# Optimization experiments

Hardware: AMD Instinct MI355X
Metric: run time of the kernel (lower is better)

## Reference

```python
import jax, jax.numpy as jnp
import numpy as np

DIM = 256
B = 8
H = 56
W = 56
K = 2
EPS = 1e-5  # torch BatchNorm2d default eps


def _conv1x1(x, w, b):
    # x: [B,C,H,W], w: [O,C], b: [O]
    return jnp.einsum('oc,bchw->bohw', w, x) + b[None, :, None, None]


def _bn(x, g, be, m, v):
    # inference-mode BatchNorm2d with running stats
    s = g / jnp.sqrt(v + EPS)
    return x * s[None, :, None, None] + (be - m * s)[None, :, None, None]


def _grapher(x, w1, b1, g1, be1, m1, v1, wg, bg, gg, beg, mg, vg, w2, b2, g2, be2, m2, v2):
    # fc1: 1x1 conv + BN
    h = _bn(_conv1x1(x, w1, b1), g1, be1, m1, v1)
    Hh, Ww = h.shape[2], h.shape[3]
    # MRConv4d: running max over circular-shift differences
    # torch.cat([x[:,:,-i:,:], x[:,:,:-i,:]], dim=2) == jnp.roll(x, i, axis=2)
    xj = jnp.zeros_like(h)

    def body_h(c, i):
        return jnp.maximum(c, h - jnp.roll(h, i, axis=2)), None

    xj, _ = jax.lax.scan(body_h, xj, jnp.arange(K, Hh, K))

    def body_w(c, i):
        return jnp.maximum(c, h - jnp.roll(h, i, axis=3)), None

    xj, _ = jax.lax.scan(body_w, xj, jnp.arange(K, Ww, K))

    cat = jnp.concatenate([h, xj], axis=1)  # [B, 2*dim, H, W]
    # MRConv4d.nn: Conv2d(2*dim, 2*dim, 1) -> BN(2*dim) -> GELU (exact erf)
    g = jax.nn.gelu(_bn(_conv1x1(cat, wg, bg), gg, beg, mg, vg), approximate=False)
    # fc2: Conv2d(2*dim, dim, 1) + BN(dim), then residual
    return _bn(_conv1x1(g, w2, b2), g2, be2, m2, v2) + x


def setup_inputs() -> dict:
    key = jax.random.key(0)
    ks = jax.random.split(key, 12)
    d, d2 = DIM, 2 * DIM

    def w(k, o, c):
        return jax.random.normal(k, (o, c), jnp.float32) * np.float32(1.0 / np.sqrt(c))

    return {
        'x': jax.random.normal(ks[0], (B, d, H, W), jnp.float32),
        'w1': w(ks[1], d, d), 'b1': jnp.zeros((d,), jnp.float32),
        'g1': jnp.ones((d,), jnp.float32), 'be1': jnp.zeros((d,), jnp.float32),
        'm1': jax.random.normal(ks[2], (d,), jnp.float32) * 0.1,
        'v1': jax.random.uniform(ks[3], (d,), jnp.float32, 0.5, 1.5),
        'wg': w(ks[4], d2, d2), 'bg': jnp.zeros((d2,), jnp.float32),
        'gg': jnp.ones((d2,), jnp.float32), 'beg': jnp.zeros((d2,), jnp.float32),
        'mg': jax.random.normal(ks[5], (d2,), jnp.float32) * 0.1,
        'vg': jax.random.uniform(ks[6], (d2,), jnp.float32, 0.5, 1.5),
        'w2': w(ks[7], d, d2), 'b2': jnp.zeros((d,), jnp.float32),
        'g2': jnp.ones((d,), jnp.float32), 'be2': jnp.zeros((d,), jnp.float32),
        'm2': jax.random.normal(ks[8], (d,), jnp.float32) * 0.1,
        'v2': jax.random.uniform(ks[9], (d,), jnp.float32, 0.5, 1.5),
    }


def reference(x, w1, b1, g1, be1, m1, v1, wg, bg, gg, beg, mg, vg, w2, b2, g2, be2, m2, v2):
    return _grapher(x, w1, b1, g1, be1, m1, v1, wg, bg, gg, beg, mg, vg, w2, b2, g2, be2, m2, v2)
```

## Files before the change

### kernel.cpp

```cpp
#include <hip/hip_runtime.h>
#include <math.h>

#define SPB 3136
#define NB 8
#define MTOT (NB*SPB)
#define EPS 1e-5f
#define XT_LD  288
#define CAT_LD 544

typedef unsigned short u16;
typedef __attribute__((ext_vector_type(8))) short short8;
typedef __attribute__((ext_vector_type(4))) float float4v;

__device__ __forceinline__ float b2f(u16 v){ unsigned u=((unsigned)v)<<16; float f; __builtin_memcpy(&f,&u,4); return f; }
__device__ __forceinline__ u16 f2b(float f){ unsigned u; __builtin_memcpy(&u,&f,4); u += 0x7fffu + ((u>>16)&1u); return (u16)(u>>16); }
__device__ __forceinline__ float gelu_f(float z){
  float t = 1.5957691216f * z * (1.0f + 0.044715f*z*z);
  return __fdividef(z, 1.0f + __expf(-t));
}

__device__ __forceinline__ void gll16(const u16* g, u16* l){
  __builtin_amdgcn_global_load_lds((const __attribute__((address_space(1))) void*)g,
                                   (__attribute__((address_space(3))) void*)l, 16, 0, 0);
}

__global__ void prep_k(const float* __restrict__ x, u16* __restrict__ xt,
                       const float* __restrict__ w1,const float* __restrict__ wg,const float* __restrict__ w2,
                       const float* b1,const float* g1,const float* be1,const float* m1,const float* v1,
                       const float* bg,const float* gg,const float* beg,const float* mg,const float* vg,
                       const float* b2,const float* g2,const float* be2,const float* m2,const float* v2,
                       u16* __restrict__ w1b,u16* __restrict__ wgb,u16* __restrict__ w2b,float* cst){
  __shared__ float t[32][33];
  if (blockIdx.z < 8) {
    int b = blockIdx.z, ct = blockIdx.y, st = blockIdx.x;
    int ts = threadIdx.x, tc = threadIdx.y;
    #pragma unroll
    for (int i=0;i<4;i++){
      int c = tc + i*8;
      t[c][ts] = x[((size_t)(b*256 + ct*32 + c))*SPB + st*32 + ts];
    }
    __syncthreads();
    #pragma unroll
    for (int i=0;i<4;i++){
      int r = tc + i*8;
      xt[((size_t)(b*SPB + st*32 + r))*XT_LD + ct*32 + ts] = f2b(t[ts][r]);
    }
  } else {
    int tid = threadIdx.y*32 + threadIdx.x;
    int w = ((blockIdx.z-8)*8 + blockIdx.y)*98 + blockIdx.x;
    int i = w*256 + tid;
    if (i < 65536)  w1b[(i>>8)*XT_LD  + (i&255)] = f2b(w1[i]);
    if (i < 262144) wgb[(i>>9)*CAT_LD + (i&511)] = f2b(wg[i]);
    if (i < 131072) w2b[(i>>9)*CAT_LD + (i&511)] = f2b(w2[i]);
    if (i < 256) {
      float s = g1[i]*rsqrtf(v1[i]+EPS);
      cst[i] = s; cst[256+i] = b1[i]*s + be1[i] - m1[i]*s;
      float s2 = g2[i]*rsqrtf(v2[i]+EPS);
      cst[1536+i] = s2; cst[1792+i] = b2[i]*s2 + be2[i] - m2[i]*s2;
    }
    if (i < 512) {
      float s = gg[i]*rsqrtf(vg[i]+EPS);
      cst[512+i] = s; cst[1024+i] = bg[i]*s + beg[i] - mg[i]*s;
    }
  }
}

__global__ __launch_bounds__(256) void minmax_k(const u16* __restrict__ cat, float* __restrict__ rmin, float* __restrict__ cmin){
  __shared__ float red[8][256];
  int b = blockIdx.x/56, i = blockIdx.x%56;
  int col = blockIdx.y;
  int slice = threadIdx.x >> 5;
  int c0 = (threadIdx.x & 31) * 8;
  const u16* base; size_t stride;
  if (!col){ base = cat + ((size_t)(b*SPB + i*56))*CAT_LD + c0; stride = CAT_LD; }
  else     { base = cat + ((size_t)(b*SPB + i))*CAT_LD + c0;    stride = (size_t)56*CAT_LD; }
  float m[8];
  #pragma unroll
  for (int k=0;k<8;k++) m[k]=3.4e38f;
  #pragma unroll
  for (int jj=0;jj<7;jj++){
    short8 v = *(const short8*)(base + (size_t)(slice + jj*8)*stride);
    #pragma unroll
    for (int k=0;k<8;k++) m[k] = fminf(m[k], b2f((u16)v[k]));
  }
  #pragma unroll
  for (int k=0;k<8;k++) red[slice][c0+k] = m[k];
  __syncthreads();
  int t = threadIdx.x;
  if (t < 64){
    int par = t >> 5;
    int cc = (t & 31) * 8;
    float* out = col ? cmin : rmin;
    float* p = &out[((size_t)(b*2+par)*56 + i)*256 + cc];
    #pragma unroll
    for (int k=0;k<8;k++)
      p[k] = fminf(fminf(red[par][cc+k], red[par+2][cc+k]),
                   fminf(red[par+4][cc+k], red[par+6][cc+k]));
  }
}

__global__ __launch_bounds__(256) void xj_k(u16* __restrict__ cat, const float* __restrict__ rmin, const float* __restrict__ cmin){
  int b = blockIdx.y;
  int t = threadIdx.x;
  int s = blockIdx.x*8 + (t>>5);
  int c0 = (t&31)*8;
  int y = s/56, x = s%56;
  size_t idx = ((size_t)(b*SPB + s))*CAT_LD;
  short8 h8 = *(const short8*)&cat[idx + c0];
  const float* cp = &cmin[((size_t)(b*2+(y&1))*56 + x)*256 + c0];
  const float* rp = &rmin[((size_t)(b*2+(x&1))*56 + y)*256 + c0];
  float4v cv0 = *(const float4v*)cp, cv1 = *(const float4v*)(cp+4);
  float4v rv0 = *(const float4v*)rp, rv1 = *(const float4v*)(rp+4);
  short8 o;
  #pragma unroll
  for (int j=0;j<8;j++){
    float cm = (j<4) ? cv0[j] : cv1[j-4];
    float rm = (j<4) ? rv0[j] : rv1[j-4];
    o[j] = (short)f2b(fmaxf(0.0f, b2f((u16)h8[j]) - fminf(cm, rm)));
  }
  *(short8*)&cat[idx + 256 + c0] = o;
}

__device__ __forceinline__ int xcd_remap(int orig, int nwg){
  int q = nwg >> 3, r = nwg & 7, xc = orig & 7, rest = orig >> 3;
  int base = (xc < r) ? xc*(q+1) : r*(q+1) + (xc-r)*q;
  return base + rest;
}

template<int KTOT, int LDA, int LDB, int EPI>
__global__ __launch_bounds__(256,2) void gemm_k(
    const u16* __restrict__ Ain, const u16* __restrict__ Wt,
    const float* __restrict__ scale, const float* __restrict__ bias,
    void* __restrict__ outp, const float* __restrict__ resid)
{
  __shared__ __align__(16) u16 smem[36864];
  const int tid = threadIdx.x;
  const int nwg = gridDim.x * gridDim.y;
  const int flat = blockIdx.y * gridDim.x + blockIdx.x;
  const int s_ = xcd_remap(flat, nwg);
  const int m0 = (s_ / gridDim.y) * 256;
  const int o0 = (s_ % gridDim.y) * 128;
  const int lane = tid & 63, wid = tid >> 6;
  const int quad = lane >> 4, l16 = lane & 15;

  float4v acc[4][8];
  #pragma unroll
  for (int i=0;i<4;i++)
    #pragma unroll
    for (int j=0;j<8;j++) acc[i][j] = (float4v){0.f,0.f,0.f,0.f};

  const int row = tid >> 2;
  const int q8s = ((tid & 3) ^ ((tid >> 3) & 3)) * 8;
  const u16* ga0 = Ain + ((size_t)(m0 + row))*LDA + q8s;
  const u16* gb0 = Wt  + ((size_t)(o0 + row))*LDB + q8s;
  u16* l8 = smem + tid*8;

  auto STAGE = [&](int kt, int buf){
    u16* b_ = l8 + buf*12288;
    gll16(ga0 + kt,                     b_);
    gll16(ga0 + (size_t) 64*LDA + kt,   b_ + 2048);
    gll16(ga0 + (size_t)128*LDA + kt,   b_ + 4096);
    gll16(ga0 + (size_t)192*LDA + kt,   b_ + 6144);
    gll16(gb0 + kt,                     b_ + 8192);
    gll16(gb0 + (size_t) 64*LDB + kt,   b_ + 10240);
  };
  const int swz = (l16 >> 1) & 3;
  auto COMPUTE = [&](int buf){
    const u16* A_ = smem + buf*12288;
    const u16* B_ = A_ + 8192;
    const int kq = (quad ^ swz) * 8;
    short8 af[4], bfr[8];
    #pragma unroll
    for (int im=0;im<4;im++) af[im]  = *(const short8*)&A_[(wid*64+im*16+l16)*32 + kq];
    #pragma unroll
    for (int in=0;in<8;in++) bfr[in] = *(const short8*)&B_[(in*16+l16)*32 + kq];
    #pragma unroll
    for (int im=0;im<4;im++)
      #pragma unroll
      for (int in=0;in<8;in++)
        acc[im][in] = __builtin_amdgcn_mfma_f32_16x16x32_bf16(af[im], bfr[in], acc[im][in], 0, 0, 0);
  };

  constexpr int NIT = KTOT / 32;
  STAGE(0, 0);
  STAGE(32, 1);
  #pragma unroll
  for (int t = 0; t < NIT; ++t) {
    __builtin_amdgcn_sched_barrier(0);
    if (t + 1 < NIT) asm volatile("s_waitcnt vmcnt(6) lgkmcnt(0)" ::: "memory");
    else             asm volatile("s_waitcnt vmcnt(0) lgkmcnt(0)" ::: "memory");
    __builtin_amdgcn_s_barrier();
    __builtin_amdgcn_sched_barrier(0);
    if (t + 2 < NIT) STAGE((t+2)*32, (t+2)%3);
    COMPUTE(t%3);
  }
  __syncthreads();

  if (EPI == 1 || EPI == 2) {
    u16* tile = smem;
    #pragma unroll
    for (int im=0;im<4;im++)
      #pragma unroll
      for (int in=0;in<8;in++){
        int ol = in*16 + l16;
        float sc = scale[o0+ol], bi = bias[o0+ol];
        #pragma unroll
        for (int r=0;r<4;r++){
          float v = acc[im][in][r]*sc + bi;
          if (EPI==2) v = gelu_f(v);
          tile[(wid*64+im*16+quad*4+r)*128 + ol] = f2b(v);
        }
      }
    __syncthreads();
    u16* op = (u16*)outp;
    #pragma unroll
    for (int p=0;p<16;p++){
      int chunk = p*256 + tid;
      int rr = chunk >> 4, off = (chunk & 15)*8;
      *(uint4*)&op[((size_t)(m0 + rr))*CAT_LD + o0 + off] = *(const uint4*)&tile[rr*128 + off];
    }
  } else {
    float* ftile = (float*)smem;
    float* op = (float*)outp;
    #pragma unroll
    for (int h=0; h<2; h++){
      #pragma unroll
      for (int im=0;im<4;im++)
        #pragma unroll
        for (int in4=0;in4<4;in4++){
          int in = h*4 + in4;
          int c64 = in4*16 + l16;
          int og = o0 + h*64 + c64;
          float sc = scale[og], bi = bias[og];
          float4v v;
          #pragma unroll
          for (int r=0;r<4;r++) v[r] = acc[im][in][r]*sc + bi;
          *(float4v*)&ftile[c64*260 + wid*64 + im*16 + quad*4] = v;
        }
      __syncthreads();
      #pragma unroll
      for (int p=0;p<16;p++){
        int chunk = p*256 + tid;
        int rr = chunk >> 6, off = (chunk & 63)*4;
        int m = m0 + off;
        int b = m / SPB, s = m - b*SPB;
        size_t g = ((size_t)(b*256 + o0 + h*64 + rr))*SPB + s;
        float4v v = *(const float4v*)&ftile[rr*260 + off];
        v.x += resid[g]; v.y += resid[g+1]; v.z += resid[g+2]; v.w += resid[g+3];
        *(float4v*)&op[g] = v;
      }
      __syncthreads();
    }
  }
}

extern "C" void kernel_launch(void* const* d_in, const int* in_sizes, int n_in,
                              void* d_out, int out_size, void* d_ws, size_t ws_size,
                              hipStream_t stream)
{
  const float* x  = (const float*)d_in[0];
  const float* w1 = (const float*)d_in[1];
  const float* b1 = (const float*)d_in[2];
  const float* g1 = (const float*)d_in[3];
  const float* be1= (const float*)d_in[4];
  const float* m1 = (const float*)d_in[5];
  const float* v1 = (const float*)d_in[6];
  const float* wg = (const float*)d_in[7];
  const float* bg = (const float*)d_in[8];
  const float* gg = (const float*)d_in[9];
  const float* beg= (const float*)d_in[10];
  const float* mg = (const float*)d_in[11];
  const float* vg = (const float*)d_in[12];
  const float* w2 = (const float*)d_in[13];
  const float* b2 = (const float*)d_in[14];
  const float* g2 = (const float*)d_in[15];
  const float* be2= (const float*)d_in[16];
  const float* m2 = (const float*)d_in[17];
  const float* v2 = (const float*)d_in[18];

  char* ws = (char*)d_ws;
  size_t off = 0;
  auto alloc = [&](size_t bytes){ void* p = ws + off; off += (bytes + 255) & ~(size_t)255; return p; };
  u16* xt    = (u16*)alloc((size_t)MTOT*XT_LD*2);
  u16* catt  = (u16*)alloc((size_t)MTOT*CAT_LD*2);
  u16* gt    = (u16*)alloc((size_t)MTOT*CAT_LD*2);
  u16* w1b   = (u16*)alloc((size_t)256*XT_LD*2);
  u16* wgb   = (u16*)alloc((size_t)512*CAT_LD*2);
  u16* w2b   = (u16*)alloc((size_t)256*CAT_LD*2);
  float* cst = (float*)alloc((size_t)2048*4);
  float* rmin= (float*)alloc((size_t)NB*2*56*256*4);
  float* cmin= (float*)alloc((size_t)NB*2*56*256*4);

  hipLaunchKernelGGL(prep_k, dim3(98,8,10), dim3(32,8), 0, stream,
                     x, xt, w1,wg,w2, b1,g1,be1,m1,v1, bg,gg,beg,mg,vg, b2,g2,be2,m2,v2,
                     w1b,wgb,w2b, cst);
  hipLaunchKernelGGL((gemm_k<256,XT_LD,XT_LD,1>), dim3(98,2), dim3(256), 0, stream,
                     xt, w1b, cst+0, cst+256, (void*)catt, (const float*)nullptr);
  hipLaunchKernelGGL(minmax_k, dim3(NB*56,2), dim3(256), 0, stream, catt, rmin, cmin);
  hipLaunchKernelGGL(xj_k, dim3(392, NB), dim3(256), 0, stream, catt, rmin, cmin);
  hipLaunchKernelGGL((gemm_k<512,CAT_LD,CAT_LD,2>), dim3(98,4), dim3(256), 0, stream,
                     catt, wgb, cst+512, cst+1024, (void*)gt, (const float*)nullptr);
  hipLaunchKernelGGL((gemm_k<512,CAT_LD,CAT_LD,3>), dim3(98,2), dim3(256), 0, stream,
                     gt, w2b, cst+1536, cst+1792, d_out, x);
}
```

Measured before the change: 179.4 us.

## Shrink GEMM tile to 128x128 with 512-thread blocks and 16-row warp slices

```diff
diff --git a/kernel.cpp b/kernel.cpp
--- a/kernel.cpp
+++ b/kernel.cpp
@@ -128,26 +128,24 @@
 }
 
 template<int KTOT, int LDA, int LDB, int EPI>
-__global__ __launch_bounds__(256,2) void gemm_k(
+__global__ __launch_bounds__(512,4) void gemm_k(
     const u16* __restrict__ Ain, const u16* __restrict__ Wt,
     const float* __restrict__ scale, const float* __restrict__ bias,
     void* __restrict__ outp, const float* __restrict__ resid)
 {
-  __shared__ __align__(16) u16 smem[36864];
+  __shared__ __align__(16) u16 smem[24576];
   const int tid = threadIdx.x;
   const int nwg = gridDim.x * gridDim.y;
   const int flat = blockIdx.y * gridDim.x + blockIdx.x;
   const int s_ = xcd_remap(flat, nwg);
-  const int m0 = (s_ / gridDim.y) * 256;
+  const int m0 = (s_ / gridDim.y) * 128;
   const int o0 = (s_ % gridDim.y) * 128;
   const int lane = tid & 63, wid = tid >> 6;
   const int quad = lane >> 4, l16 = lane & 15;
 
-  float4v acc[4][8];
-  #pragma unroll
-  for (int i=0;i<4;i++)
-    #pragma unroll
-    for (int j=0;j<8;j++) acc[i][j] = (float4v){0.f,0.f,0.f,0.f};
+  float4v acc[8];
+  #pragma unroll
+  for (int j=0;j<8;j++) acc[j] = (float4v){0.f,0.f,0.f,0.f};
 
   const int row = tid >> 2;
   const int q8s = ((tid & 3) ^ ((tid >> 3) & 3)) * 8;
@@ -156,29 +154,22 @@
   u16* l8 = smem + tid*8;
 
   auto STAGE = [&](int kt, int buf){
-    u16* b_ = l8 + buf*12288;
-    gll16(ga0 + kt,                     b_);
-    gll16(ga0 + (size_t) 64*LDA + kt,   b_ + 2048);
-    gll16(ga0 + (size_t)128*LDA + kt,   b_ + 4096);
-    gll16(ga0 + (size_t)192*LDA + kt,   b_ + 6144);
-    gll16(gb0 + kt,                     b_ + 8192);
-    gll16(gb0 + (size_t) 64*LDB + kt,   b_ + 10240);
+    u16* b_ = l8 + buf*8192;
+    gll16(ga0 + kt, b_);
+    gll16(gb0 + kt, b_ + 4096);
   };
   const int swz = (l16 >> 1) & 3;
   auto COMPUTE = [&](int buf){
-    const u16* A_ = smem + buf*12288;
-    const u16* B_ = A_ + 8192;
+    const u16* A_ = smem + buf*8192;
+    const u16* B_ = A_ + 4096;
     const int kq = (quad ^ swz) * 8;
-    short8 af[4], bfr[8];
-    #pragma unroll
-    for (int im=0;im<4;im++) af[im]  = *(const short8*)&A_[(wid*64+im*16+l16)*32 + kq];
+    short8 af = *(const short8*)&A_[(wid*16 + l16)*32 + kq];
+    short8 bfr[8];
     #pragma unroll
     for (int in=0;in<8;in++) bfr[in] = *(const short8*)&B_[(in*16+l16)*32 + kq];
     #pragma unroll
-    for (int im=0;im<4;im++)
-      #pragma unroll
-      for (int in=0;in<8;in++)
-        acc[im][in] = __builtin_amdgcn_mfma_f32_16x16x32_bf16(af[im], bfr[in], acc[im][in], 0, 0, 0);
+    for (int in=0;in<8;in++)
+      acc[in] = __builtin_amdgcn_mfma_f32_16x16x32_bf16(af, bfr[in], acc[in], 0, 0, 0);
   };
 
   constexpr int NIT = KTOT / 32;
@@ -187,7 +178,7 @@
   #pragma unroll
   for (int t = 0; t < NIT; ++t) {
     __builtin_amdgcn_sched_barrier(0);
-    if (t + 1 < NIT) asm volatile("s_waitcnt vmcnt(6) lgkmcnt(0)" ::: "memory");
+    if (t + 1 < NIT) asm volatile("s_waitcnt vmcnt(2) lgkmcnt(0)" ::: "memory");
     else             asm volatile("s_waitcnt vmcnt(0) lgkmcnt(0)" ::: "memory");
     __builtin_amdgcn_s_barrier();
     __builtin_amdgcn_sched_barrier(0);
@@ -199,23 +190,21 @@
   if (EPI == 1 || EPI == 2) {
     u16* tile = smem;
     #pragma unroll
-    for (int im=0;im<4;im++)
+    for (int in=0;in<8;in++){
+      int ol = in*16 + l16;
+      float sc = scale[o0+ol], bi = bias[o0+ol];
       #pragma unroll
-      for (int in=0;in<8;in++){
-        int ol = in*16 + l16;
-        float sc = scale[o0+ol], bi = bias[o0+ol];
-        #pragma unroll
-        for (int r=0;r<4;r++){
-          float v = acc[im][in][r]*sc + bi;
-          if (EPI==2) v = gelu_f(v);
-          tile[(wid*64+im*16+quad*4+r)*128 + ol] = f2b(v);
-        }
+      for (int r=0;r<4;r++){
+        float v = acc[in][r]*sc + bi;
+        if (EPI==2) v = gelu_f(v);
+        tile[(wid*16+quad*4+r)*128 + ol] = f2b(v);
       }
+    }
     __syncthreads();
     u16* op = (u16*)outp;
     #pragma unroll
-    for (int p=0;p<16;p++){
-      int chunk = p*256 + tid;
+    for (int p=0;p<4;p++){
+      int chunk = p*512 + tid;
       int rr = chunk >> 4, off = (chunk & 15)*8;
       *(uint4*)&op[((size_t)(m0 + rr))*CAT_LD + o0 + off] = *(const uint4*)&tile[rr*128 + off];
     }
@@ -225,27 +214,25 @@
     #pragma unroll
     for (int h=0; h<2; h++){
       #pragma unroll
-      for (int im=0;im<4;im++)
+      for (int in4=0;in4<4;in4++){
+        int in = h*4 + in4;
+        int c64 = in4*16 + l16;
+        int og = o0 + h*64 + c64;
+        float sc = scale[og], bi = bias[og];
+        float4v v;
         #pragma unroll
-        for (int in4=0;in4<4;in4++){
-          int in = h*4 + in4;
-          int c64 = in4*16 + l16;
-          int og = o0 + h*64 + c64;
-          float sc = scale[og], bi = bias[og];
-          float4v v;
-          #pragma unroll
-          for (int r=0;r<4;r++) v[r] = acc[im][in][r]*sc + bi;
-          *(float4v*)&ftile[c64*260 + wid*64 + im*16 + quad*4] = v;
-        }
+        for (int r=0;r<4;r++) v[r] = acc[in][r]*sc + bi;
+        *(float4v*)&ftile[c64*132 + wid*16 + quad*4] = v;
+      }
       __syncthreads();
       #pragma unroll
-      for (int p=0;p<16;p++){
-        int chunk = p*256 + tid;
-        int rr = chunk >> 6, off = (chunk & 63)*4;
+      for (int p=0;p<4;p++){
+        int chunk = p*512 + tid;
+        int rr = chunk >> 5, off = (chunk & 31)*4;
         int m = m0 + off;
         int b = m / SPB, s = m - b*SPB;
         size_t g = ((size_t)(b*256 + o0 + h*64 + rr))*SPB + s;
-        float4v v = *(const float4v*)&ftile[rr*260 + off];
+        float4v v = *(const float4v*)&ftile[rr*132 + off];
         v.x += resid[g]; v.y += resid[g+1]; v.z += resid[g+2]; v.w += resid[g+3];
         *(float4v*)&op[g] = v;
       }
@@ -294,12 +281,12 @@
   hipLaunchKernelGGL(prep_k, dim3(98,8,10), dim3(32,8), 0, stream,
                      x, xt, w1,wg,w2, b1,g1,be1,m1,v1, bg,gg,beg,mg,vg, b2,g2,be2,m2,v2,
                      w1b,wgb,w2b, cst);
-  hipLaunchKernelGGL((gemm_k<256,XT_LD,XT_LD,1>), dim3(98,2), dim3(256), 0, stream,
+  hipLaunchKernelGGL((gemm_k<256,XT_LD,XT_LD,1>), dim3(196,2), dim3(512), 0, stream,
                      xt, w1b, cst+0, cst+256, (void*)catt, (const float*)nullptr);
   hipLaunchKernelGGL(minmax_k, dim3(NB*56,2), dim3(256), 0, stream, catt, rmin, cmin);
   hipLaunchKernelGGL(xj_k, dim3(392, NB), dim3(256), 0, stream, catt, rmin, cmin);
-  hipLaunchKernelGGL((gemm_k<512,CAT_LD,CAT_LD,2>), dim3(98,4), dim3(256), 0, stream,
+  hipLaunchKernelGGL((gemm_k<512,CAT_LD,CAT_LD,2>), dim3(196,4), dim3(512), 0, stream,
                      catt, wgb, cst+512, cst+1024, (void*)gt, (const float*)nullptr);
-  hipLaunchKernelGGL((gemm_k<512,CAT_LD,CAT_LD,3>), dim3(98,2), dim3(256), 0, stream,
+  hipLaunchKernelGGL((gemm_k<512,CAT_LD,CAT_LD,3>), dim3(196,2), dim3(512), 0, stream,
                      gt, w2b, cst+1536, cst+1792, d_out, x);
 }
```

After: 179.6 us. About the same (+0.1%).
